# Kernel optimization log

Measured on AMD Instinct MI355X. Metric: run time of the kernel, lower is better.

The kernel has to match this reference:

```python
import jax, jax.numpy as jnp
import numpy as np

N_ANCHORS = 262144
N_GT = 100
IMG = 1024.0
N_SAMPLE = 256
POS_RATIO = 0.5
POS_T = 0.7
NEG_T = 0.3
ALLOWED_BORDER = 0.0
NUM_FG = int(POS_RATIO * N_SAMPLE)  # 128


def compute_overlap(a, g):
    """IoU between anchors a:(N,4) and gt g:(R,4), py-faster-rcnn +1 pixel convention."""
    area_a = (a[:, 2] - a[:, 0] + 1.0) * (a[:, 3] - a[:, 1] + 1.0)          # (N,)
    area_g = (g[:, 2] - g[:, 0] + 1.0) * (g[:, 3] - g[:, 1] + 1.0)          # (R,)
    iw = jnp.minimum(a[:, None, 2], g[None, :, 2]) - jnp.maximum(a[:, None, 0], g[None, :, 0]) + 1.0
    ih = jnp.minimum(a[:, None, 3], g[None, :, 3]) - jnp.maximum(a[:, None, 1], g[None, :, 1]) + 1.0
    inter = jnp.maximum(iw, 0.0) * jnp.maximum(ih, 0.0)                     # (N,R)
    return inter / (area_a[:, None] + area_g[None, :] - inter)


def bbox_transform(gt, an):
    """Encode gt boxes relative to anchors -> (dx,dy,dw,dh), shape (N,4)."""
    aw = an[:, 2] - an[:, 0] + 1.0
    ah = an[:, 3] - an[:, 1] + 1.0
    acx = an[:, 0] + 0.5 * aw
    acy = an[:, 1] + 0.5 * ah
    gw = gt[:, 2] - gt[:, 0] + 1.0
    gh = gt[:, 3] - gt[:, 1] + 1.0
    gcx = gt[:, 0] + 0.5 * gw
    gcy = gt[:, 1] + 0.5 * gh
    return jnp.stack([(gcx - acx) / aw, (gcy - acy) / ah,
                      jnp.log(gw / aw), jnp.log(gh / ah)], axis=1)


def keep_at_most(mask, k, key):
    """Keep at most k True entries of mask, chosen uniformly at random (fixed shape)."""
    r = jnp.where(mask, jax.random.uniform(key, mask.shape), jnp.inf)
    rank = jnp.argsort(jnp.argsort(r))  # rank[i] = position of i in ascending sort
    return mask & (rank < k)


def anchor_target(anchors, image_shape, gt, key):
    # anchors: (N,4), gt: (R,4)
    R = gt.shape[0]
    inside = ((anchors[:, 0] >= -ALLOWED_BORDER) & (anchors[:, 1] >= -ALLOWED_BORDER)
              & (anchors[:, 2] < ALLOWED_BORDER + image_shape[1])
              & (anchors[:, 3] < ALLOWED_BORDER + image_shape[0]))            # (N,)
    iou = compute_overlap(anchors, gt)                                        # (N,R)
    iou_m = jnp.where(inside[:, None], iou, -1.0)  # restrict to inside anchors
    max_ov = jnp.max(iou_m, axis=1)                                           # (N,)

    k1, k2, k3 = jax.random.split(key, 3)
    labels = jnp.full(anchors.shape[:1], -1.0, dtype=jnp.float32)
    # clobber_positives=False: background first
    labels = jnp.where(inside & (max_ov < NEG_T), 0.0, labels)
    # per-gt argmax anchors (tie set), randomly truncated to at most R like tf.random_shuffle[:R]
    gt_max = jnp.max(iou_m, axis=0)                                           # (R,)
    cand = jnp.any(iou_m == gt_max[None, :], axis=1) & inside                 # (N,)
    cand = keep_at_most(cand, R, k1)
    labels = jnp.where(cand, 1.0, labels)
    labels = jnp.where(inside & (max_ov >= POS_T), 1.0, labels)

    # balance: subsample positives to NUM_FG
    fg = labels == 1.0
    labels = jnp.where(fg & ~keep_at_most(fg, NUM_FG, k2), -1.0, labels)
    # subsample negatives to n_sample - n_fg
    n_fg = jnp.sum(labels == 1.0)
    bg = labels == 0.0
    labels = jnp.where(bg & ~keep_at_most(bg, N_SAMPLE - n_fg, k3), -1.0, labels)
    # umap: outside anchors stay -1
    labels = jnp.where(inside, labels, -1.0)

    # bbox targets: faithful to original tf.gather(gt, to_int32(max_overlaps))
    idx = jnp.clip(max_ov.astype(jnp.int32), 0, R - 1)
    tgt = bbox_transform(gt[idx], anchors)                                    # (N,4)
    tgt = jnp.where(inside[:, None], tgt, 0.0)  # scatter_nd at inside indices
    return labels[None], tgt[None]


def setup_inputs() -> dict:
    key = jax.random.key(0)
    k1, k2, k3, k4 = jax.random.split(key, 4)
    ctr = jax.random.uniform(k1, (N_ANCHORS, 2), minval=-64.0, maxval=IMG + 64.0)
    wh = jax.random.uniform(k2, (N_ANCHORS, 2), minval=16.0, maxval=256.0)
    anchors = jnp.concatenate([ctr - 0.5 * wh, ctr + 0.5 * wh], axis=1)
    gctr = jax.random.uniform(k3, (N_GT, 2), minval=100.0, maxval=IMG - 100.0)
    gwh = jax.random.uniform(k4, (N_GT, 2), minval=30.0, maxval=200.0)
    gt = jnp.concatenate([gctr - 0.5 * gwh, gctr + 0.5 * gwh], axis=1)
    return {"total_anchors": anchors[None],
            "image_shape": jnp.array([IMG, IMG], jnp.float32),
            "gt_boxes": gt[None]}


def reference(total_anchors, image_shape, gt_boxes):
    key = jax.random.key(42)  # original uses unseeded tf.random_shuffle
    labels, bbox_reg_targets = anchor_target(total_anchors[0], image_shape,
                                             gt_boxes[0][:, :4], key)
    return labels, bbox_reg_targets
```

## Files before the change

### kernel.cpp

```cpp
#include <hip/hip_runtime.h>
#include <stdint.h>

#define NGT_MAX 128
#define CAND_CAP 8192
#define CSEL_CAP 512
#define FILT_CAP 16384
#define SUB_CAP 2048


__host__ __device__ inline void tf2x32(uint32_t k0, uint32_t k1, uint32_t c0, uint32_t c1,
                                       uint32_t& o0, uint32_t& o1) {
  uint32_t ks[3] = {k0, k1, k0 ^ k1 ^ 0x1BD11BDAu};
  uint32_t x0 = c0 + ks[0];
  uint32_t x1 = c1 + ks[1];
  const int rot[2][4] = {{13, 15, 26, 6}, {17, 29, 16, 24}};
#pragma unroll
  for (int i = 0; i < 5; ++i) {
#pragma unroll
    for (int j = 0; j < 4; ++j) {
      x0 += x1;
      int r = rot[i & 1][j];
      x1 = (x1 << r) | (x1 >> (32 - r));
      x1 ^= x0;
    }
    x0 += ks[(i + 1) % 3];
    x1 += ks[(i + 2) % 3] + (uint32_t)(i + 1);
  }
  o0 = x0; o1 = x1;
}

__device__ inline uint64_t sel_key(uint32_t i, uint32_t ka, uint32_t kb) {
  uint32_t o0, o1;
  tf2x32(ka, kb, 0u, i, o0, o1);
  uint32_t bits = o0 ^ o1;
  return ((uint64_t)(bits >> 9) << 32) | (uint64_t)i;
}

__device__ inline uint32_t fmap(float v) {
  uint32_t u = __float_as_uint(v);
  return (u & 0x80000000u) ? ~u : (u | 0x80000000u);
}
__device__ inline float funmap(uint32_t m) {
  return (m & 0x80000000u) ? __uint_as_float(m & 0x7FFFFFFFu) : __uint_as_float(~m);
}

__device__ __forceinline__ void acc_reduce(const uint32_t* __restrict__ acc,
                                           uint32_t* sbase) {
  const int t = threadIdx.x;
  if (t < 64) {
    uint32_t f = 0u, g2 = 0u;
    if (t < 32) { f = acc[t * 16]; g2 = acc[t * 16 + 1]; }
#pragma unroll
    for (int o = 32; o > 0; o >>= 1) {
      f += __shfl_down(f, o);
      g2 += __shfl_down(g2, o);
    }
    if (t == 0) { sbase[0] = f; sbase[1] = g2; }
  }
}

__device__ inline void cons_meta(uint32_t baseF, uint32_t baseB, uint32_t* needF,
                                 uint32_t* Tf, uint32_t* needB, uint32_t* Tb) {
  *needF = (baseF > 128u) ? 1u : 0u;
  uint64_t tf = 0, tb = 0;
  if (*needF) {
    tf = (((uint64_t)(128u * 32u)) << 23) / (uint64_t)baseF;
    if (tf > (1u << 23)) tf = (1u << 23);
  }
  uint32_t nfgmin = baseF < 128u ? baseF : 128u;
  uint32_t kbgmax = 256u - nfgmin;
  *needB = (baseB > 8192u + kbgmax) ? 1u : 0u;
  if (*needB) {
    tb = (((uint64_t)(kbgmax * 32u)) << 23) / (uint64_t)(baseB - 8192u);
    if (tb > (1u << 23)) tb = (1u << 23);
  }
  *Tf = (uint32_t)tf;
  *Tb = (uint32_t)tb;
}

__device__ __forceinline__ float iou_ref(const float4& a, float area_a, const float4& gb,
                                         float area_g) {
#pragma clang fp contract(off)
  float iw = fminf(a.z, gb.z) - fmaxf(a.x, gb.x) + 1.0f;
  float ih = fminf(a.w, gb.w) - fmaxf(a.y, gb.y) + 1.0f;
  float inter = fmaxf(iw, 0.0f) * fmaxf(ih, 0.0f);
  return inter / (area_a + area_g - inter);
}

__device__ __forceinline__ float4 tgt_ref(const float4& a, const float4& gb) {
#pragma clang fp contract(off)
  float aw = a.z - a.x + 1.0f;
  float ah = a.w - a.y + 1.0f;
  float acx = a.x + 0.5f * aw;
  float acy = a.y + 0.5f * ah;
  float gw = gb.z - gb.x + 1.0f;
  float gh = gb.w - gb.y + 1.0f;
  float gcx = gb.x + 0.5f * gw;
  float gcy = gb.y + 0.5f * gh;
  return make_float4((gcx - acx) / aw, (gcy - acy) / ah, logf(gw / aw), logf(gh / ah));
}

__global__ void __launch_bounds__(256)
k_main(const float4* __restrict__ anc, const float* __restrict__ img,
       const float4* __restrict__ gt, int N, int R,
       uint32_t* __restrict__ pmax, uint32_t* __restrict__ gmaxu,
       float* __restrict__ LBL, float4* __restrict__ TGT,
       uint32_t* __restrict__ acc) {
  __shared__ float4 sgt[NGT_MAX];
  __shared__ float sarea[NGT_MAX];
  __shared__ float sq[16 * 101];
  __shared__ uint32_t scnt[2];
  const int t = threadIdx.x, b = blockIdx.x;
  if (t < 2) scnt[t] = 0u;
  if (t < R) {
    float4 g = gt[t];
    sgt[t] = g;
    {
#pragma clang fp contract(off)
      sarea[t] = (g.z - g.x + 1.0f) * (g.w - g.y + 1.0f);
    }
  }
  for (int j = t; j < 16 * 101; j += 256) sq[j] = -1.0f;
  __syncthreads();
  const int lane = t & 63, wid = t >> 6;
  const int h = lane >> 5;
  const int al = lane & 31;
  const int p = lane & 3;
  const int i = b * 128 + wid * 32 + al;
  const int gbase = 50 * h;
  const int Rh = R - gbase;
  const float H = img[0], W = img[1];
  float4 a = anc[i];
  bool inside = (a.x >= 0.0f) && (a.y >= 0.0f) && (a.z < W) && (a.w < H);
  float area_a;
  {
#pragma clang fp contract(off)
    area_a = (a.z - a.x + 1.0f) * (a.w - a.y + 1.0f);
  }
  if (!inside) area_a = __uint_as_float(0x7FC00000u);
  const bool b1 = (p == 1), b2 = (p == 2), b3 = (p == 3);
  float part[13];
  float vmax = -1.0f;
#pragma unroll
  for (int s = 0; s < 13; ++s) {
    float v2q[4];
#pragma unroll
    for (int k = 0; k < 4; ++k) {
      const int j = 4 * s + k;
      if (j < 50 && j < Rh) {
        const int g = gbase + j;
        float4 gb = sgt[g];
        float v = iou_ref(a, area_a, gb, sarea[g]);
        vmax = fmaxf(vmax, v);
        int d1 = __builtin_amdgcn_mov_dpp(__float_as_int(v), 0xB1, 0xF, 0xF, true);
        float v1 = fmaxf(v, __int_as_float(d1));
        int d2 = __builtin_amdgcn_mov_dpp(__float_as_int(v1), 0x4E, 0xF, 0xF, true);
        v2q[k] = fmaxf(v1, __int_as_float(d2));
      } else {
        v2q[k] = -1.0f;
      }
    }
    float pp = v2q[0];
    pp = b1 ? v2q[1] : pp;
    pp = b2 ? v2q[2] : pp;
    pp = b3 ? v2q[3] : pp;
    part[s] = pp;
  }
  vmax = fmaxf(vmax, __shfl_xor(vmax, 32));
  float lbl = -1.0f;
  if (inside) {
    if (vmax < 0.3f) lbl = 0.0f;
    if (vmax >= 0.7f) lbl = 1.0f;
  }
  unsigned long long bf = __ballot(lbl == 1.0f) & 0xFFFFFFFFull;
  unsigned long long bb = __ballot(lbl == 0.0f) & 0xFFFFFFFFull;
  if (lane == 0) {
    atomicAdd(&scnt[0], (uint32_t)__popcll(bf));
    atomicAdd(&scnt[1], (uint32_t)__popcll(bb));
  }
  if (h == 0) {
    LBL[i] = lbl;
    float4 o = make_float4(0.f, 0.f, 0.f, 0.f);
    if (inside) {
      int idx = (int)vmax;
      idx = idx < 0 ? 0 : (idx > R - 1 ? R - 1 : idx);
      o = tgt_ref(a, sgt[idx]);
    }
    TGT[i] = o;
  }
#pragma unroll
  for (int s = 0; s < 13; ++s) {
    float v = part[s];
    int x = __builtin_amdgcn_mov_dpp(__float_as_int(v), 0x114, 0xF, 0xF, true);
    v = fmaxf(v, __int_as_float(x));
    x = __builtin_amdgcn_mov_dpp(__float_as_int(v), 0x118, 0xF, 0xF, true);
    v = fmaxf(v, __int_as_float(x));
    part[s] = v;
  }
  const int r = t >> 4;
  if ((t & 15) >= 12) {
#pragma unroll
    for (int s = 0; s < 13; ++s) {
      const int j = 4 * s + p;
      if (j < 50 && j < Rh) sq[r * 101 + gbase + j] = part[s];
    }
  }
  __syncthreads();
  if (t < R) {
    float m = -1.0f;
#pragma unroll 8
    for (int r2 = 0; r2 < 16; ++r2) m = fmaxf(m, sq[r2 * 101 + t]);
    uint32_t u = fmap(m);
    pmax[b * R + t] = u;
    if (u > gmaxu[t]) atomicMax(&gmaxu[t], u);
  }
  if (t == 0) {
    const uint32_t slot = (uint32_t)(b & 31) * 16u;
    atomicAdd(&acc[slot], scnt[0]);
    atomicAdd(&acc[slot + 1], scnt[1]);
  }
}

__global__ void __launch_bounds__(256)
k_gather(const float4* __restrict__ anc, const float* __restrict__ img,
         const float4* __restrict__ gt, int N, int R,
         const uint32_t* __restrict__ pmax, const uint32_t* __restrict__ gmaxu,
         float* __restrict__ LBL,
         uint64_t* __restrict__ candList, uint32_t* __restrict__ candLbl,
         uint64_t* __restrict__ listF, uint64_t* __restrict__ listB,
         uint32_t* __restrict__ counters, const uint32_t* __restrict__ acc,
         uint32_t k1a, uint32_t k1b, uint32_t k2a, uint32_t k2b,
         uint32_t k3a, uint32_t k3b) {
  __shared__ int tg[NGT_MAX];
  __shared__ float tgm[NGT_MAX];
  __shared__ float4 sgt[NGT_MAX];
  __shared__ float sarea[NGT_MAX];
  __shared__ uint64_t cbuf[256];
  __shared__ uint32_t cbufL[256];
  __shared__ uint64_t bufF[256], bufB[256];
  __shared__ uint32_t sbase[2];
  __shared__ uint32_t cC, cF, cB, oC, oF, oB;
  __shared__ int tcnt;
  const int t = threadIdx.x, b = blockIdx.x;
  if (t == 0) { tcnt = 0; cC = 0u; cF = 0u; cB = 0u; }
  acc_reduce(acc, sbase);
  if (t < R) {
    float4 g = gt[t];
    sgt[t] = g;
    {
#pragma clang fp contract(off)
      sarea[t] = (g.z - g.x + 1.0f) * (g.w - g.y + 1.0f);
    }
  }
  __syncthreads();
  const uint32_t baseF = sbase[0];
  const uint32_t baseB = sbase[1];
  uint32_t needF, Tf, needB, Tb;
  cons_meta(baseF, baseB, &needF, &Tf, &needB, &Tb);
  if (t < R) {
    uint32_t gm = gmaxu[t];
    uint32_t pm0 = pmax[(2 * b) * R + t];
    uint32_t pm1 = pmax[(2 * b + 1) * R + t];
    if (pm0 == gm || pm1 == gm) {
      int pp = atomicAdd(&tcnt, 1);
      tg[pp] = t;
      tgm[pp] = funmap(gm);
    }
  }
  __syncthreads();
  const int C0 = tcnt;
  const int i = b * 256 + t;
  const float H = img[0], W = img[1];
  float old = LBL[i];
  bool isc = false;
  if (C0 > 0) {
    float4 a = anc[i];
    bool inside = (a.x >= 0.0f) && (a.y >= 0.0f) && (a.z < W) && (a.w < H);
    if (inside) {
      float area_a;
      {
#pragma clang fp contract(off)
        area_a = (a.z - a.x + 1.0f) * (a.w - a.y + 1.0f);
      }
      for (int j = 0; j < C0; ++j) {
        int g = tg[j];
        float v = iou_ref(a, area_a, sgt[g], sarea[g]);
        isc = isc || (v == tgm[j]);
      }
    }
  }
  if (isc) {
    uint32_t code = (old == 1.0f) ? 2u : ((old == 0.0f) ? 1u : 0u);
    uint32_t pp = atomicAdd(&cC, 1u);
    cbuf[pp] = sel_key((uint32_t)i, k1a, k1b);
    cbufL[pp] = code;
  }
  float l1 = isc ? 1.0f : old;
  float out = l1;
  if (l1 == 1.0f) {
    uint64_t key = sel_key((uint32_t)i, k2a, k2b);
    if (needF && (uint32_t)(key >> 32) >= Tf) {
      out = -1.0f;
    } else {
      uint32_t pp = atomicAdd(&cF, 1u);
      bufF[pp] = key;
    }
  } else if (l1 == 0.0f) {
    uint64_t key = sel_key((uint32_t)i, k3a, k3b);
    if (needB && (uint32_t)(key >> 32) >= Tb) {
      out = -1.0f;
    } else {
      uint32_t pp = atomicAdd(&cB, 1u);
      bufB[pp] = key;
    }
  }
  LBL[i] = out;
  __syncthreads();
  if (t == 0 && cC) oC = atomicAdd(&counters[0], cC);
  if (t == 64 && cF) oF = atomicAdd(&counters[4], cF);
  if (t == 128 && cB) oB = atomicAdd(&counters[5], cB);
  __syncthreads();
  for (uint32_t j = t; j < cC; j += 256) {
    uint32_t pp = oC + j;
    if (pp < CAND_CAP) { candList[pp] = cbuf[j]; candLbl[pp] = cbufL[j]; }
  }
  for (uint32_t j = t; j < cF; j += 256) {
    uint32_t pp = oF + j;
    if (pp < FILT_CAP) listF[pp] = bufF[j];
  }
  for (uint32_t j = t; j < cB; j += 256) {
    uint32_t pp = oB + j;
    if (pp < FILT_CAP) listB[pp] = bufB[j];
  }
}

__device__ __forceinline__ void do_select(const uint64_t* list, uint32_t Mf, uint32_t k,
                                          uint32_t T, float* LBL, uint32_t* h,
                                          uint32_t* c0, uint32_t* c1, uint64_t* sub,
                                          uint32_t* scal, const uint32_t* drop,
                                          uint32_t nd) {
  const int t = threadIdx.x;
  if (Mf <= k) return;
  int bl = (T > 1u) ? (32 - __clz(T - 1u)) : 0;
  int shift = bl > 8 ? bl - 8 : 0;
  h[t] = 0u;
  if (t == 0) { scal[0] = 0u; scal[1] = 0u; scal[2] = 0u; }
  __syncthreads();
  for (uint32_t j = t; j < Mf; j += 256) {
    uint64_t key = list[j];
    bool skip = false;
    for (uint32_t d = 0; d < nd; ++d) skip = skip || (drop[d] == (uint32_t)key);
    if (!skip) atomicAdd(&h[((uint32_t)(key >> 32)) >> shift], 1u);
  }
  __syncthreads();
  c0[t] = h[t];
  __syncthreads();
  uint32_t* s = c0;
  uint32_t* d2 = c1;
  for (int dd = 1; dd < 256; dd <<= 1) {
    uint32_t v = s[t];
    if (t >= dd) v += s[t - dd];
    d2[t] = v;
    __syncthreads();
    uint32_t* tmp = s; s = d2; d2 = tmp;
  }
  uint32_t inc = s[t];
  uint32_t exc = inc - h[t];
  if (exc < k && inc >= k) { scal[1] = (uint32_t)t; scal[2] = k - exc; }
  __syncthreads();
  const uint32_t binb = scal[1], rneed = scal[2];
  for (uint32_t j = t; j < Mf; j += 256) {
    uint64_t key = list[j];
    bool skip = false;
    for (uint32_t d = 0; d < nd; ++d) skip = skip || (drop[d] == (uint32_t)key);
    if (skip) continue;
    uint32_t bin = ((uint32_t)(key >> 32)) >> shift;
    if (bin > binb) {
      LBL[(uint32_t)key] = -1.0f;
    } else if (bin == binb) {
      uint32_t pp = atomicAdd(&scal[0], 1u);
      if (pp < SUB_CAP) sub[pp] = key;
    }
  }
  __syncthreads();
  uint32_t c = scal[0] < SUB_CAP ? scal[0] : SUB_CAP;
  for (uint32_t s2 = t; s2 < c; s2 += 256) {
    uint64_t key = sub[s2];
    uint32_t rank = 0u;
    for (uint32_t j = 0; j < c; ++j) rank += (sub[j] < key) ? 1u : 0u;
    if (rank >= rneed) LBL[(uint32_t)key] = -1.0f;
  }
  __syncthreads();
}

__global__ void __launch_bounds__(256)
k_sel(float* __restrict__ LBL, uint64_t* __restrict__ listF,
      uint64_t* __restrict__ listB, const uint64_t* __restrict__ candList,
      const uint32_t* __restrict__ candLbl,
      uint32_t* __restrict__ counters, const uint32_t* __restrict__ acc, int R,
      uint32_t k3a, uint32_t k3b) {
  __shared__ uint64_t ck[CSEL_CAP];
  __shared__ uint32_t cc[CSEL_CAP];
  __shared__ uint32_t drop[256];
  __shared__ uint32_t h[256], c0s[256], c1s[256];
  __shared__ uint64_t sub[SUB_CAP];
  __shared__ uint32_t scal[8];
  __shared__ uint32_t sbase[2];
  const int t = threadIdx.x;
  if (t < 8) scal[t] = 0u;
  acc_reduce(acc, sbase);
  uint32_t C = counters[0];
  if (C > CSEL_CAP) C = CSEL_CAP;
  for (uint32_t s = t; s < C; s += 256) { ck[s] = candList[s]; cc[s] = candLbl[s]; }
  __syncthreads();
  const uint32_t baseF = sbase[0];
  const uint32_t baseB = sbase[1];
  uint32_t needFc, TfC, needBc, TbC;
  cons_meta(baseF, baseB, &needFc, &TfC, &needBc, &TbC);
  const uint32_t MfB0 = counters[5] < FILT_CAP ? counters[5] : FILT_CAP;
  for (uint32_t e = t; e < C; e += 256) {
    uint64_t key = ck[e];
    bool keep = true;
    if (C > (uint32_t)R) {
      uint32_t rank = 0;
      for (uint32_t j = 0; j < C; ++j) rank += (ck[j] < key) ? 1u : 0u;
      keep = (rank < (uint32_t)R);
    }
    uint32_t code = cc[e];
    uint32_t idx = (uint32_t)key;
    if (keep) {
      if (code != 2u) atomicAdd(&scal[4], 1u);
      if (code == 1u) atomicAdd(&scal[5], 1u);
    } else if (code != 2u) {
      uint32_t pp = atomicAdd(&scal[3], 1u);
      if (pp < 256) drop[pp] = idx;
      if (code == 0u) {
        LBL[idx] = -1.0f;
      } else {
        uint64_t key3 = sel_key(idx, k3a, k3b);
        if (needBc && (uint32_t)(key3 >> 32) >= TbC) {
          LBL[idx] = -1.0f;
        } else {
          uint32_t qq = atomicAdd(&scal[6], 1u);
          if (MfB0 + qq < FILT_CAP) listB[MfB0 + qq] = key3;
          LBL[idx] = 0.0f;
        }
      }
    }
  }
  __syncthreads();
  const uint32_t fgflips = scal[4], bgflips = scal[5];
  const uint32_t nDrop = scal[3] < 256u ? scal[3] : 256u;
  const uint32_t nAdd = scal[6];
  const uint32_t M1 = baseF + fgflips;
  const uint32_t M2 = baseB - bgflips;
  const uint32_t nfg = M1 < 128u ? M1 : 128u;
  const uint32_t kbg = 256u - nfg;
  if (M1 > 128u) {
    uint32_t MfF = counters[4] < FILT_CAP ? counters[4] : FILT_CAP;
    uint32_t TF = needFc ? TfC : (1u << 23);
    do_select(listF, MfF, 128u, TF, LBL, h, c0s, c1s, sub, scal, drop, nDrop);
  }
  if (M2 > kbg) {
    uint32_t MfB = MfB0 + nAdd;
    if (MfB > FILT_CAP) MfB = FILT_CAP;
    uint32_t TB = needBc ? TbC : (1u << 23);
    do_select(listB, MfB, kbg, TB, LBL, h, c0s, c1s, sub, scal, drop, 0u);
  }
}

extern "C" void kernel_launch(void* const* d_in, const int* in_sizes, int n_in,
                              void* d_out, int out_size, void* d_ws, size_t ws_size,
                              hipStream_t stream) {
  (void)n_in; (void)out_size; (void)ws_size;
  const int N = in_sizes[0] / 4;
  const int R = in_sizes[2] / 4;
  const int NBm = N / 128;
  const int NBg = N / 256;
  const float4* anc = (const float4*)d_in[0];
  const float* img = (const float*)d_in[1];
  const float4* gtb = (const float4*)d_in[2];
  float* LBL = (float*)d_out;
  float4* TGT = (float4*)((float*)d_out + N);

  uint8_t* ws = (uint8_t*)d_ws;
  uint32_t* counters = (uint32_t*)ws;
  uint32_t* gmaxu = (uint32_t*)(ws + 512);
  uint32_t* accum = (uint32_t*)(ws + 1024);
  uint32_t* candLbl = (uint32_t*)(ws + 16384);
  uint32_t* pmax = (uint32_t*)(ws + 65536);
  size_t off = 65536 + (size_t)NBm * R * 4;
  off = (off + 7) & ~(size_t)7;
  uint64_t* candList = (uint64_t*)(ws + off);
  uint64_t* listF = (uint64_t*)(ws + off + CAND_CAP * 8);
  uint64_t* listB = (uint64_t*)(ws + off + CAND_CAP * 8 + FILT_CAP * 8);

  uint32_t k1a, k1b, k2a, k2b, k3a, k3b;
  tf2x32(0u, 42u, 0u, 0u, k1a, k1b);
  tf2x32(0u, 42u, 0u, 1u, k2a, k2b);
  tf2x32(0u, 42u, 0u, 2u, k3a, k3b);

  hipMemsetAsync(ws, 0, 4096, stream);
  k_main<<<NBm, 256, 0, stream>>>(anc, img, gtb, N, R, pmax, gmaxu, LBL, TGT, accum);
  k_gather<<<NBg, 256, 0, stream>>>(anc, img, gtb, N, R, pmax, gmaxu, LBL,
                                    candList, candLbl, listF, listB, counters, accum,
                                    k1a, k1b, k2a, k2b, k3a, k3b);
  k_sel<<<1, 256, 0, stream>>>(LBL, listF, listB, candList, candLbl, counters, accum,
                               R, k3a, k3b);
}
```

Baseline: 139.2 us.

## Process two anchors per thread in IoU kernel to reuse GT loads

Each thread of the main IoU kernel now handles two anchors, so every GT box and area read from shared memory feeds two IoU computations. The per-GT DPP max reductions run on the max of both anchors, which halves shuffle work and block count. The per-block partial max array shrinks to one row per 256 anchors, so the follow-up kernel reads a single pmax entry instead of two. Padding GT entries up to NGT_MAX with degenerate boxes removes the R bound checks from the inner loop. In exchange, register pressure rises and there are fewer blocks to hide latency.

```diff
diff --git a/kernel.cpp b/kernel.cpp
--- a/kernel.cpp
+++ b/kernel.cpp
@@ -112,12 +112,12 @@
   __shared__ uint32_t scnt[2];
   const int t = threadIdx.x, b = blockIdx.x;
   if (t < 2) scnt[t] = 0u;
-  if (t < R) {
-    float4 g = gt[t];
+  if (t < NGT_MAX) {
+    float4 g = (t < R) ? gt[t] : make_float4(0.0f, 0.0f, -1.0f, -1.0f);
     sgt[t] = g;
     {
 #pragma clang fp contract(off)
-      sarea[t] = (g.z - g.x + 1.0f) * (g.w - g.y + 1.0f);
+      sarea[t] = (t < R) ? ((g.z - g.x + 1.0f) * (g.w - g.y + 1.0f)) : 0.0f;
     }
   }
   for (int j = t; j < 16 * 101; j += 256) sq[j] = -1.0f;
@@ -126,36 +126,44 @@
   const int h = lane >> 5;
   const int al = lane & 31;
   const int p = lane & 3;
-  const int i = b * 128 + wid * 32 + al;
+  const int i0 = b * 256 + wid * 64 + al;
+  const int i1 = i0 + 32;
   const int gbase = 50 * h;
-  const int Rh = R - gbase;
   const float H = img[0], W = img[1];
-  float4 a = anc[i];
-  bool inside = (a.x >= 0.0f) && (a.y >= 0.0f) && (a.z < W) && (a.w < H);
-  float area_a;
+  float4 a0 = anc[i0];
+  float4 a1 = anc[i1];
+  bool in0 = (a0.x >= 0.0f) && (a0.y >= 0.0f) && (a0.z < W) && (a0.w < H);
+  bool in1 = (a1.x >= 0.0f) && (a1.y >= 0.0f) && (a1.z < W) && (a1.w < H);
+  float ar0, ar1;
   {
 #pragma clang fp contract(off)
-    area_a = (a.z - a.x + 1.0f) * (a.w - a.y + 1.0f);
-  }
-  if (!inside) area_a = __uint_as_float(0x7FC00000u);
+    ar0 = (a0.z - a0.x + 1.0f) * (a0.w - a0.y + 1.0f);
+    ar1 = (a1.z - a1.x + 1.0f) * (a1.w - a1.y + 1.0f);
+  }
+  if (!in0) ar0 = __uint_as_float(0x7FC00000u);
+  if (!in1) ar1 = __uint_as_float(0x7FC00000u);
   const bool b1 = (p == 1), b2 = (p == 2), b3 = (p == 3);
   float part[13];
-  float vmax = -1.0f;
+  float vm0 = -1.0f, vm1 = -1.0f;
 #pragma unroll
   for (int s = 0; s < 13; ++s) {
     float v2q[4];
 #pragma unroll
     for (int k = 0; k < 4; ++k) {
       const int j = 4 * s + k;
-      if (j < 50 && j < Rh) {
+      if (j < 50) {
         const int g = gbase + j;
         float4 gb = sgt[g];
-        float v = iou_ref(a, area_a, gb, sarea[g]);
-        vmax = fmaxf(vmax, v);
+        float ag = sarea[g];
+        float v0 = iou_ref(a0, ar0, gb, ag);
+        float v1 = iou_ref(a1, ar1, gb, ag);
+        vm0 = fmaxf(vm0, v0);
+        vm1 = fmaxf(vm1, v1);
+        float v = fmaxf(v0, v1);
         int d1 = __builtin_amdgcn_mov_dpp(__float_as_int(v), 0xB1, 0xF, 0xF, true);
-        float v1 = fmaxf(v, __int_as_float(d1));
-        int d2 = __builtin_amdgcn_mov_dpp(__float_as_int(v1), 0x4E, 0xF, 0xF, true);
-        v2q[k] = fmaxf(v1, __int_as_float(d2));
+        float v1q = fmaxf(v, __int_as_float(d1));
+        int d2 = __builtin_amdgcn_mov_dpp(__float_as_int(v1q), 0x4E, 0xF, 0xF, true);
+        v2q[k] = fmaxf(v1q, __int_as_float(d2));
       } else {
         v2q[k] = -1.0f;
       }
@@ -166,27 +174,42 @@
     pp = b3 ? v2q[3] : pp;
     part[s] = pp;
   }
-  vmax = fmaxf(vmax, __shfl_xor(vmax, 32));
-  float lbl = -1.0f;
-  if (inside) {
-    if (vmax < 0.3f) lbl = 0.0f;
-    if (vmax >= 0.7f) lbl = 1.0f;
-  }
-  unsigned long long bf = __ballot(lbl == 1.0f) & 0xFFFFFFFFull;
-  unsigned long long bb = __ballot(lbl == 0.0f) & 0xFFFFFFFFull;
+  vm0 = fmaxf(vm0, __shfl_xor(vm0, 32));
+  vm1 = fmaxf(vm1, __shfl_xor(vm1, 32));
+  float lbl0 = -1.0f, lbl1 = -1.0f;
+  if (in0) {
+    if (vm0 < 0.3f) lbl0 = 0.0f;
+    if (vm0 >= 0.7f) lbl0 = 1.0f;
+  }
+  if (in1) {
+    if (vm1 < 0.3f) lbl1 = 0.0f;
+    if (vm1 >= 0.7f) lbl1 = 1.0f;
+  }
+  uint32_t nf = (uint32_t)__popcll(__ballot(lbl0 == 1.0f) & 0xFFFFFFFFull)
+              + (uint32_t)__popcll(__ballot(lbl1 == 1.0f) & 0xFFFFFFFFull);
+  uint32_t nb = (uint32_t)__popcll(__ballot(lbl0 == 0.0f) & 0xFFFFFFFFull)
+              + (uint32_t)__popcll(__ballot(lbl1 == 0.0f) & 0xFFFFFFFFull);
   if (lane == 0) {
-    atomicAdd(&scnt[0], (uint32_t)__popcll(bf));
-    atomicAdd(&scnt[1], (uint32_t)__popcll(bb));
+    atomicAdd(&scnt[0], nf);
+    atomicAdd(&scnt[1], nb);
   }
   if (h == 0) {
-    LBL[i] = lbl;
-    float4 o = make_float4(0.f, 0.f, 0.f, 0.f);
-    if (inside) {
-      int idx = (int)vmax;
+    LBL[i0] = lbl0;
+    LBL[i1] = lbl1;
+    float4 o0 = make_float4(0.f, 0.f, 0.f, 0.f);
+    float4 o1 = make_float4(0.f, 0.f, 0.f, 0.f);
+    if (in0) {
+      int idx = (int)vm0;
       idx = idx < 0 ? 0 : (idx > R - 1 ? R - 1 : idx);
-      o = tgt_ref(a, sgt[idx]);
-    }
-    TGT[i] = o;
+      o0 = tgt_ref(a0, sgt[idx]);
+    }
+    if (in1) {
+      int idx = (int)vm1;
+      idx = idx < 0 ? 0 : (idx > R - 1 ? R - 1 : idx);
+      o1 = tgt_ref(a1, sgt[idx]);
+    }
+    TGT[i0] = o0;
+    TGT[i1] = o1;
   }
 #pragma unroll
   for (int s = 0; s < 13; ++s) {
@@ -202,7 +225,7 @@
 #pragma unroll
     for (int s = 0; s < 13; ++s) {
       const int j = 4 * s + p;
-      if (j < 50 && j < Rh) sq[r * 101 + gbase + j] = part[s];
+      if (j < 50) sq[r * 101 + gbase + j] = part[s];
     }
   }
   __syncthreads();
@@ -259,9 +282,7 @@
   cons_meta(baseF, baseB, &needF, &Tf, &needB, &Tb);
   if (t < R) {
     uint32_t gm = gmaxu[t];
-    uint32_t pm0 = pmax[(2 * b) * R + t];
-    uint32_t pm1 = pmax[(2 * b + 1) * R + t];
-    if (pm0 == gm || pm1 == gm) {
+    if (pmax[b * R + t] == gm) {
       int pp = atomicAdd(&tcnt, 1);
       tg[pp] = t;
       tgm[pp] = funmap(gm);
@@ -475,7 +496,7 @@
   (void)n_in; (void)out_size; (void)ws_size;
   const int N = in_sizes[0] / 4;
   const int R = in_sizes[2] / 4;
-  const int NBm = N / 128;
+  const int NBm = N / 256;
   const int NBg = N / 256;
   const float4* anc = (const float4*)d_in[0];
   const float* img = (const float*)d_in[1];
```

Result: faster. 129.1 us (-7.3%).
